# Optimization experiments

Measured on AMD Instinct MI355X. Metric: run time of the kernel, lower is better.

The kernel has to match this reference:

```python
import jax, jax.numpy as jnp
import numpy as np
from jax.scipy.special import gammaln

ADIM, ODIM = 256, 80
B, T_TEXT, T_FEATS = 4, 160, 800


def conv1d(x, w, b, pad):
    # x: (B, C_in, T), w: (C_out, C_in, K)
    y = jax.lax.conv_general_dilated(x, w, (1,), [(pad, pad)],
                                     dimension_numbers=('NCH', 'OIH', 'NCH'))
    return y + b[None, :, None]


def betaln(x, y):
    return gammaln(x) + gammaln(y) - gammaln(x + y)


def beta_binomial_prior(T, N, w=1.0):
    # Matches scipy betabinom.logpmf(k, N, alpha, beta) with
    # alpha = w*arange(1, T+1), beta = w*(T - alpha + 1), k = arange(N).
    a = w * jnp.arange(1, T + 1, dtype=jnp.float32)          # (T,)
    b = w * (T - a + 1.0)                                    # (T,)
    k = jnp.arange(N, dtype=jnp.float32)[:, None]            # (N, 1)
    Nf = jnp.float32(N)
    logp = (gammaln(Nf + 1.0) - gammaln(k + 1.0) - gammaln(Nf - k + 1.0)
            + betaln(k + a, Nf - k + b) - betaln(a, b))      # (N, T)
    return logp.T                                            # (T_feats, T_text)


def setup_inputs() -> dict:
    key = jax.random.key(0)
    ks = jax.random.split(key, 12)
    s = 0.05
    return {
        'text': jax.random.normal(ks[0], (B, T_TEXT, ADIM), jnp.float32),
        'feats': jax.random.normal(ks[1], (B, T_FEATS, ODIM), jnp.float32),
        'text_lengths': jnp.full((B,), T_TEXT, dtype=jnp.int32),
        'feats_lengths': jnp.full((B,), T_FEATS, dtype=jnp.int32),
        'x_masks': jnp.zeros((B, T_TEXT), dtype=bool),
        't_w1': jax.random.normal(ks[2], (ADIM, ADIM, 3), jnp.float32) * s,
        't_b1': jnp.zeros((ADIM,), jnp.float32),
        't_w2': jax.random.normal(ks[3], (ADIM, ADIM, 1), jnp.float32) * s,
        't_b2': jnp.zeros((ADIM,), jnp.float32),
        'f_w1': jax.random.normal(ks[4], (ADIM, ODIM, 3), jnp.float32) * s,
        'f_b1': jnp.zeros((ADIM,), jnp.float32),
        'f_w2': jax.random.normal(ks[5], (ADIM, ADIM, 3), jnp.float32) * s,
        'f_b2': jnp.zeros((ADIM,), jnp.float32),
        'f_w3': jax.random.normal(ks[6], (ADIM, ADIM, 1), jnp.float32) * s,
        'f_b3': jnp.zeros((ADIM,), jnp.float32),
    }


def reference(text, feats, text_lengths, feats_lengths, x_masks,
              t_w1, t_b1, t_w2, t_b2, f_w1, f_b1, f_w2, f_b2, f_w3, f_b3):
    # text conv stem: (B, T_text, adim) -> (B, T_text, adim)
    t = jnp.swapaxes(text, 1, 2)
    t = jax.nn.relu(conv1d(t, t_w1, t_b1, 1))
    t = conv1d(t, t_w2, t_b2, 0)
    t = jnp.swapaxes(t, 1, 2)
    # feats conv stem: (B, T_feats, odim) -> (B, T_feats, adim)
    f = jnp.swapaxes(feats, 1, 2)
    f = jax.nn.relu(conv1d(f, f_w1, f_b1, 1))
    f = jax.nn.relu(conv1d(f, f_w2, f_b2, 1))
    f = conv1d(f, f_w3, f_b3, 0)
    f = jnp.swapaxes(f, 1, 2)
    # L2-distance score: (B, T_feats, T_text)
    diff = f[:, :, None, :] - t[:, None, :, :]               # (B,Tf,Tt,adim)
    score = -jnp.sqrt(jnp.sum(diff * diff, axis=-1))
    score = jnp.where(x_masks[:, None, :], -jnp.inf, score)
    log_p_attn = jax.nn.log_softmax(score, axis=-1)
    # beta-binomial prior (lengths == max, so prior fills the whole matrix)
    prior = beta_binomial_prior(feats.shape[1], text.shape[1])
    return log_p_attn + prior[None, :, :]
```

## Files before the change

kernel.cpp:

```cpp
#include <hip/hip_runtime.h>
#include <math.h>

#define NB 4
#define TTEXT 160
#define TFEAT 800

typedef __bf16 bf16x8 __attribute__((ext_vector_type(8)));
typedef float f32x4 __attribute__((ext_vector_type(4)));

__device__ inline unsigned short f2bf(float f) {
    unsigned int u = __builtin_bit_cast(unsigned int, f);
    unsigned int r = u + 0x7fffu + ((u >> 16) & 1u);
    return (unsigned short)(r >> 16);
}
__device__ inline float bf2f(unsigned short h) {
    unsigned int u = ((unsigned int)h) << 16;
    return __builtin_bit_cast(float, u);
}

__global__ __launch_bounds__(256) void prep_kernel(
    const float* __restrict__ tw1, const float* __restrict__ tw2,
    const float* __restrict__ fw1, const float* __restrict__ fw2,
    const float* __restrict__ fw3,
    unsigned short* __restrict__ wb_t1, unsigned short* __restrict__ wb_t2,
    unsigned short* __restrict__ wb_f1, unsigned short* __restrict__ wb_f2,
    unsigned short* __restrict__ wb_f3, float* __restrict__ lg)
{
    const int u = blockIdx.x * 256 + threadIdx.x;
    if (u >= 598016) {
        const int n = u - 598016;
        if (n < 1024) lg[n] = (n >= 1) ? (float)lgamma((double)n) : 0.0f;
        return;
    }
    int rem = u;
    int CIN, CINP, K; const float* src; unsigned short* dst;
    if (rem < 196608)                  { CIN = 256; CINP = 256; K = 3; src = tw1; dst = wb_t1; }
    else if ((rem -= 196608) < 65536)  { CIN = 256; CINP = 256; K = 1; src = tw2; dst = wb_t2; }
    else if ((rem -= 65536) < 73728)   { CIN = 80;  CINP = 96;  K = 3; src = fw1; dst = wb_f1; }
    else if ((rem -= 73728) < 196608)  { CIN = 256; CINP = 256; K = 3; src = fw2; dst = wb_f2; }
    else { rem -= 196608;                CIN = 256; CINP = 256; K = 1; src = fw3; dst = wb_f3; }
    const int q = rem & 31, coc = rem >> 5, co = coc & 255, c = coc >> 8;
    const int cpk = CINP / 32, k = c / cpk, ci = (c % cpk) * 32 + q;
    const float v = (ci < CIN) ? src[((size_t)co * CIN + ci) * K + k] : 0.0f;
    dst[rem] = f2bf(v);
}

__global__ __launch_bounds__(512) void stems_kernel(
    const float* __restrict__ text, const float* __restrict__ feats,
    const unsigned short* __restrict__ wt1, const float* __restrict__ bt1,
    const unsigned short* __restrict__ wt2, const float* __restrict__ bt2,
    const unsigned short* __restrict__ wf1, const float* __restrict__ bf1v,
    const unsigned short* __restrict__ wf2, const float* __restrict__ bf2v,
    const unsigned short* __restrict__ wf3, const float* __restrict__ bf3v,
    unsigned short* __restrict__ tB, float* __restrict__ tnorm,
    unsigned short* __restrict__ fC, float* __restrict__ fnorm)
{
    __shared__ __align__(16) unsigned short s[11056];
    __shared__ float s_red[16][8];
    const int tid = threadIdx.x;
    const int w  = tid >> 6;
    const int l  = tid & 63;
    const int lr = l & 15;
    const int lk = l >> 4;
    const int co0 = w * 32;
    const int koff = lk * 8;
    const int bid = blockIdx.x;

    if (bid < 40) {
        const int b  = bid & 3;
        const int t0 = (bid >> 2) << 4;
        unsigned short* s_in  = s;
        unsigned short* s_mid = s + 4752;

        for (int idx = tid; idx < 18 * 64; idx += 512) {
            const int r = idx >> 6, c4 = idx & 63;
            const int x = t0 - 1 + r;
            float4 v = {0.f, 0.f, 0.f, 0.f};
            if (x >= 0 && x < TTEXT)
                v = *(const float4*)(text + ((size_t)(b * TTEXT + x)) * 256 + c4 * 4);
            unsigned short* p = s_in + r * 264 + c4 * 4;
            p[0] = f2bf(v.x); p[1] = f2bf(v.y); p[2] = f2bf(v.z); p[3] = f2bf(v.w);
        }
        __syncthreads();

        f32x4 acc[2];
#pragma unroll
        for (int n = 0; n < 2; ++n) acc[n] = {0.f, 0.f, 0.f, 0.f};
#pragma unroll 8
        for (int c = 0; c < 24; ++c) {
            const int k  = c >> 3;
            const int ci = ((c & 7) << 5) + koff;
            const bf16x8 a = *(const bf16x8*)(s_in + (lr + k) * 264 + ci);
#pragma unroll
            for (int n = 0; n < 2; ++n) {
                const bf16x8 bb = *(const bf16x8*)(wt1 + (((size_t)c * 256 + co0 + n * 16 + lr) << 5) + koff);
                acc[n] = __builtin_amdgcn_mfma_f32_16x16x32_bf16(a, bb, acc[n], 0, 0, 0);
            }
        }
#pragma unroll
        for (int n = 0; n < 2; ++n) {
            const float bv = bt1[co0 + n * 16 + lr];
#pragma unroll
            for (int r = 0; r < 4; ++r)
                s_mid[(lk * 4 + r) * 264 + co0 + n * 16 + lr] = f2bf(fmaxf(acc[n][r] + bv, 0.f));
        }
        __syncthreads();

        f32x4 a2[2];
#pragma unroll
        for (int n = 0; n < 2; ++n) a2[n] = {0.f, 0.f, 0.f, 0.f};
#pragma unroll
        for (int c = 0; c < 8; ++c) {
            const bf16x8 a = *(const bf16x8*)(s_mid + lr * 264 + (c << 5) + koff);
#pragma unroll
            for (int n = 0; n < 2; ++n) {
                const bf16x8 bb = *(const bf16x8*)(wt2 + (((size_t)c * 256 + co0 + n * 16 + lr) << 5) + koff);
                a2[n] = __builtin_amdgcn_mfma_f32_16x16x32_bf16(a, bb, a2[n], 0, 0, 0);
            }
        }
        float bv2[2];
#pragma unroll
        for (int n = 0; n < 2; ++n) bv2[n] = bt2[co0 + n * 16 + lr];
#pragma unroll
        for (int r = 0; r < 4; ++r) {
            const int row = lk * 4 + r;
            float np = 0.f;
#pragma unroll
            for (int n = 0; n < 2; ++n) {
                const unsigned short h = f2bf(a2[n][r] + bv2[n]);
                tB[((size_t)(b * TTEXT + t0 + row)) * 256 + co0 + n * 16 + lr] = h;
                const float vq = bf2f(h);
                np = fmaf(vq, vq, np);
            }
            np += __shfl_xor(np, 1);
            np += __shfl_xor(np, 2);
            np += __shfl_xor(np, 4);
            np += __shfl_xor(np, 8);
            if (lr == 0) s_red[row][w] = np;
        }
        __syncthreads();
        if (tid < 16) {
            float s4 = 0.f;
#pragma unroll
            for (int ww = 0; ww < 8; ++ww) s4 += s_red[tid][ww];
            tnorm[b * TTEXT + t0 + tid] = s4;
        }
    } else {
        const int fb = bid - 40;
        const int b  = fb & 3;
        const int t0 = (fb >> 2) << 4;
        unsigned short* s_fin = s;
        unsigned short* s_b1  = s + 2080;
        unsigned short* s_b2  = s + 6832;

        for (int idx = tid; idx < 20 * 24; idx += 512) {
            const int r  = idx / 24, c4 = idx - r * 24;
            const int ch = c4 * 4;
            const int x  = t0 - 2 + r;
            float4 v = {0.f, 0.f, 0.f, 0.f};
            if (ch < 80 && x >= 0 && x < TFEAT)
                v = *(const float4*)(feats + ((size_t)(b * TFEAT + x)) * 80 + ch);
            unsigned short* p = s_fin + r * 104 + ch;
            p[0] = f2bf(v.x); p[1] = f2bf(v.y); p[2] = f2bf(v.z); p[3] = f2bf(v.w);
        }
        __syncthreads();

        f32x4 acc1[2][2];
#pragma unroll
        for (int m = 0; m < 2; ++m)
#pragma unroll
            for (int n = 0; n < 2; ++n) acc1[m][n] = {0.f, 0.f, 0.f, 0.f};
#pragma unroll
        for (int c = 0; c < 9; ++c) {
            const int k  = c / 3;
            const int ci = (c - k * 3) * 32 + koff;
            bf16x8 a[2];
#pragma unroll
            for (int m = 0; m < 2; ++m) {
                int rr = m * 16 + lr + k;
                if (rr > 19) rr = 19;
                a[m] = *(const bf16x8*)(s_fin + rr * 104 + ci);
            }
#pragma unroll
            for (int n = 0; n < 2; ++n) {
                const bf16x8 bb = *(const bf16x8*)(wf1 + (((size_t)c * 256 + co0 + n * 16 + lr) << 5) + koff);
                acc1[0][n] = __builtin_amdgcn_mfma_f32_16x16x32_bf16(a[0], bb, acc1[0][n], 0, 0, 0);
                acc1[1][n] = __builtin_amdgcn_mfma_f32_16x16x32_bf16(a[1], bb, acc1[1][n], 0, 0, 0);
            }
        }
#pragma unroll
        for (int n = 0; n < 2; ++n) {
            const float bv = bf1v[co0 + n * 16 + lr];
#pragma unroll
            for (int m = 0; m < 2; ++m)
#pragma unroll
                for (int r = 0; r < 4; ++r) {
                    const int i = m * 16 + lk * 4 + r;
                    if (i < 18)
                        s_b1[i * 264 + co0 + n * 16 + lr] = f2bf(fmaxf(acc1[m][n][r] + bv, 0.f));
                }
        }
        __syncthreads();

        f32x4 acc2[2];
#pragma unroll
        for (int n = 0; n < 2; ++n) acc2[n] = {0.f, 0.f, 0.f, 0.f};
#pragma unroll 8
        for (int c = 0; c < 24; ++c) {
            const int k  = c >> 3;
            const int ci = ((c & 7) << 5) + koff;
            const bf16x8 a = *(const bf16x8*)(s_b1 + (lr + k) * 264 + ci);
#pragma unroll
            for (int n = 0; n < 2; ++n) {
                const bf16x8 bb = *(const bf16x8*)(wf2 + (((size_t)c * 256 + co0 + n * 16 + lr) << 5) + koff);
                acc2[n] = __builtin_amdgcn_mfma_f32_16x16x32_bf16(a, bb, acc2[n], 0, 0, 0);
            }
        }
#pragma unroll
        for (int n = 0; n < 2; ++n) {
            const float bv = bf2v[co0 + n * 16 + lr];
#pragma unroll
            for (int r = 0; r < 4; ++r)
                s_b2[(lk * 4 + r) * 264 + co0 + n * 16 + lr] = f2bf(fmaxf(acc2[n][r] + bv, 0.f));
        }
        __syncthreads();

        f32x4 a3[2];
#pragma unroll
        for (int n = 0; n < 2; ++n) a3[n] = {0.f, 0.f, 0.f, 0.f};
#pragma unroll
        for (int c = 0; c < 8; ++c) {
            const bf16x8 a = *(const bf16x8*)(s_b2 + lr * 264 + (c << 5) + koff);
#pragma unroll
            for (int n = 0; n < 2; ++n) {
                const bf16x8 bb = *(const bf16x8*)(wf3 + (((size_t)c * 256 + co0 + n * 16 + lr) << 5) + koff);
                a3[n] = __builtin_amdgcn_mfma_f32_16x16x32_bf16(a, bb, a3[n], 0, 0, 0);
            }
        }
        float bv3[2];
#pragma unroll
        for (int n = 0; n < 2; ++n) bv3[n] = bf3v[co0 + n * 16 + lr];
#pragma unroll
        for (int r = 0; r < 4; ++r) {
            const int row = lk * 4 + r;
            float np = 0.f;
#pragma unroll
            for (int n = 0; n < 2; ++n) {
                const unsigned short h = f2bf(a3[n][r] + bv3[n]);
                fC[((size_t)(b * TFEAT + t0 + row)) * 256 + co0 + n * 16 + lr] = h;
                const float vq = bf2f(h);
                np = fmaf(vq, vq, np);
            }
            np += __shfl_xor(np, 1);
            np += __shfl_xor(np, 2);
            np += __shfl_xor(np, 4);
            np += __shfl_xor(np, 8);
            if (lr == 0) s_red[row][w] = np;
        }
        __syncthreads();
        if (tid < 16) {
            float s4 = 0.f;
#pragma unroll
            for (int ww = 0; ww < 8; ++ww) s4 += s_red[tid][ww];
            fnorm[b * TFEAT + t0 + tid] = s4;
        }
    }
}

__global__ __launch_bounds__(256) void score_mfma(
    const unsigned short* __restrict__ F, const unsigned short* __restrict__ Tt,
    const float* __restrict__ fnorm, const float* __restrict__ tnorm,
    const unsigned char* __restrict__ xmask, const float* __restrict__ lg,
    float* __restrict__ out)
{
    const int b  = blockIdx.y;
    const int tid = threadIdx.x;
    const int w  = tid >> 6;
    const int l  = tid & 63;
    const int lr = l & 15;
    const int lk = l >> 4;
    const int i0 = blockIdx.x * 16;
    const int nstart = (w < 2) ? w * 3 : 6 + (w - 2) * 2;
    const int ncnt   = (w < 2) ? 3 : 2;

    __shared__ float s_red[16][4];
    __shared__ float s_red2[16][4];

    f32x4 acc[3];
#pragma unroll
    for (int ni = 0; ni < 3; ++ni) acc[ni] = {0.f, 0.f, 0.f, 0.f};

    const unsigned short* __restrict__ Fp = F + ((size_t)(b * TFEAT + i0 + lr)) * 256;
    const unsigned short* __restrict__ Tp = Tt + ((size_t)b * TTEXT) * 256;

#pragma unroll
    for (int c = 0; c < 8; ++c) {
        const int d = c * 32 + lk * 8;
        const bf16x8 a = *(const bf16x8*)(Fp + d);
#pragma unroll
        for (int ni = 0; ni < 3; ++ni) {
            if (ni < ncnt) {
                const int n = nstart + ni;
                const bf16x8 bb = *(const bf16x8*)(Tp + ((size_t)(n * 16 + lr)) * 256 + d);
                acc[ni] = __builtin_amdgcn_mfma_f32_16x16x32_bf16(a, bb, acc[ni], 0, 0, 0);
            }
        }
    }

    float fn[4];
#pragma unroll
    for (int r = 0; r < 4; ++r) fn[r] = fnorm[b * TFEAT + i0 + lk * 4 + r];
    float tn[3]; bool mk[3];
#pragma unroll
    for (int ni = 0; ni < 3; ++ni) {
        const int j = (nstart + ni) * 16 + lr;
        if (ni < ncnt) {
            tn[ni] = tnorm[b * TTEXT + j];
            mk[ni] = xmask[b * TTEXT + j] != 0;
        } else { tn[ni] = 0.f; mk[ni] = true; }
    }
    float sc[3][4];
#pragma unroll
    for (int ni = 0; ni < 3; ++ni)
#pragma unroll
        for (int r = 0; r < 4; ++r) {
            const float d2 = fn[r] + tn[ni] - 2.0f * acc[ni][r];
            const float sv = -sqrtf(fmaxf(d2, 0.0f));
            sc[ni][r] = mk[ni] ? -INFINITY : sv;
        }

#pragma unroll
    for (int r = 0; r < 4; ++r) {
        float mx = sc[0][r];
#pragma unroll
        for (int ni = 1; ni < 3; ++ni) mx = fmaxf(mx, sc[ni][r]);
        mx = fmaxf(mx, __shfl_xor(mx, 1));
        mx = fmaxf(mx, __shfl_xor(mx, 2));
        mx = fmaxf(mx, __shfl_xor(mx, 4));
        mx = fmaxf(mx, __shfl_xor(mx, 8));
        if (lr == 0) s_red[lk * 4 + r][w] = mx;
    }
    __syncthreads();
    float gmax[4];
#pragma unroll
    for (int r = 0; r < 4; ++r) {
        const int row = lk * 4 + r;
        gmax[r] = fmaxf(fmaxf(s_red[row][0], s_red[row][1]),
                        fmaxf(s_red[row][2], s_red[row][3]));
        float sm = 0.f;
#pragma unroll
        for (int ni = 0; ni < 3; ++ni)
            if (ni < ncnt) sm += expf(sc[ni][r] - gmax[r]);
        sm += __shfl_xor(sm, 1);
        sm += __shfl_xor(sm, 2);
        sm += __shfl_xor(sm, 4);
        sm += __shfl_xor(sm, 8);
        if (lr == 0) s_red2[row][w] = sm;
    }
    __syncthreads();

    const float cst = lg[161] - lg[961] + lg[801];
#pragma unroll
    for (int r = 0; r < 4; ++r) {
        const int row = lk * 4 + r;
        const float lse = gmax[r] + logf(s_red2[row][0] + s_red2[row][1]
                                       + s_red2[row][2] + s_red2[row][3]);
        const int grow = i0 + row;
        const float rowterm = cst - lg[grow + 1] - lg[801 - grow];
#pragma unroll
        for (int ni = 0; ni < 3; ++ni) {
            if (ni < ncnt) {
                const int j = (nstart + ni) * 16 + lr;
                const float prior = rowterm - lg[j + 1] - lg[160 - j]
                                  + lg[grow + j + 1] + lg[960 - grow - j];
                out[((size_t)(b * TFEAT + grow)) * TTEXT + j] = sc[ni][r] - lse + prior;
            }
        }
    }
}

extern "C" void kernel_launch(void* const* d_in, const int* in_sizes, int n_in,
                              void* d_out, int out_size, void* d_ws, size_t ws_size,
                              hipStream_t stream) {
    const float* text  = (const float*)d_in[0];
    const float* feats = (const float*)d_in[1];
    const unsigned char* xmask = (const unsigned char*)d_in[4];
    const float* t_w1 = (const float*)d_in[5];
    const float* t_b1 = (const float*)d_in[6];
    const float* t_w2 = (const float*)d_in[7];
    const float* t_b2 = (const float*)d_in[8];
    const float* f_w1 = (const float*)d_in[9];
    const float* f_b1 = (const float*)d_in[10];
    const float* f_w2 = (const float*)d_in[11];
    const float* f_b2 = (const float*)d_in[12];
    const float* f_w3 = (const float*)d_in[13];
    const float* f_b3 = (const float*)d_in[14];
    float* out = (float*)d_out;

    char* wp = (char*)d_ws;
    auto alloc = [&](size_t bytes) -> void* {
        void* p = wp; wp += (bytes + 255) & ~(size_t)255; return p;
    };
    float* lg = (float*)alloc(1024 * 4);
    unsigned short* wb_t1 = (unsigned short*)alloc(196608 * 2);
    unsigned short* wb_t2 = (unsigned short*)alloc(65536 * 2);
    unsigned short* wb_f1 = (unsigned short*)alloc(73728 * 2);
    unsigned short* wb_f2 = (unsigned short*)alloc(196608 * 2);
    unsigned short* wb_f3 = (unsigned short*)alloc(65536 * 2);
    unsigned short* tB = (unsigned short*)alloc((size_t)NB * TTEXT * 256 * 2);
    unsigned short* fC = (unsigned short*)alloc((size_t)NB * TFEAT * 256 * 2);
    float* fnorm = (float*)alloc((size_t)NB * TFEAT * 4);
    float* tnorm = (float*)alloc((size_t)NB * TTEXT * 4);

    prep_kernel<<<2340, 256, 0, stream>>>(
        t_w1, t_w2, f_w1, f_w2, f_w3, wb_t1, wb_t2, wb_f1, wb_f2, wb_f3, lg);

    stems_kernel<<<240, 512, 0, stream>>>(
        text, feats,
        wb_t1, t_b1, wb_t2, t_b2,
        wb_f1, f_b1, wb_f2, f_b2, wb_f3, f_b3,
        tB, tnorm, fC, fnorm);

    score_mfma<<<dim3(50, NB), 256, 0, stream>>>(fC, tB, fnorm, tnorm, xmask, lg, out);
}
```

Before: 35.92 us.

## Fuse score computation into stems kernel with per-batch spin-wait flags

Merges the score/log-softmax kernel into the stems kernel. Each feats block keeps its projected features and norms in shared memory and waits on a per-batch atomic counter until the 10 text blocks for that batch have published tB and tnorm. This removes one kernel launch and the global round trip for fC and fnorm. The cost is a spin-wait that only works if all 240 blocks are co-resident; otherwise it can deadlock or stall.

```diff
diff --git a/kernel.cpp b/kernel.cpp
--- a/kernel.cpp
+++ b/kernel.cpp
@@ -24,8 +24,10 @@
     const float* __restrict__ fw3,
     unsigned short* __restrict__ wb_t1, unsigned short* __restrict__ wb_t2,
     unsigned short* __restrict__ wb_f1, unsigned short* __restrict__ wb_f2,
-    unsigned short* __restrict__ wb_f3, float* __restrict__ lg)
+    unsigned short* __restrict__ wb_f3, float* __restrict__ lg,
+    int* __restrict__ flags)
 {
+    if (blockIdx.x == 0 && threadIdx.x < 16) flags[threadIdx.x] = 0;
     const int u = blockIdx.x * 256 + threadIdx.x;
     if (u >= 598016) {
         const int n = u - 598016;
@@ -45,18 +47,22 @@
     dst[rem] = f2bf(v);
 }
 
-__global__ __launch_bounds__(512) void stems_kernel(
+__global__ __launch_bounds__(512) void fused_kernel(
     const float* __restrict__ text, const float* __restrict__ feats,
+    const unsigned char* __restrict__ xmask,
     const unsigned short* __restrict__ wt1, const float* __restrict__ bt1,
     const unsigned short* __restrict__ wt2, const float* __restrict__ bt2,
     const unsigned short* __restrict__ wf1, const float* __restrict__ bf1v,
     const unsigned short* __restrict__ wf2, const float* __restrict__ bf2v,
     const unsigned short* __restrict__ wf3, const float* __restrict__ bf3v,
+    const float* __restrict__ lg,
     unsigned short* __restrict__ tB, float* __restrict__ tnorm,
-    unsigned short* __restrict__ fC, float* __restrict__ fnorm)
+    int* __restrict__ flags, float* __restrict__ out)
 {
     __shared__ __align__(16) unsigned short s[11056];
     __shared__ float s_red[16][8];
+    __shared__ float s_red2[16][8];
+    __shared__ float s_fn[16];
     const int tid = threadIdx.x;
     const int w  = tid >> 6;
     const int l  = tid & 63;
@@ -145,162 +151,154 @@
             for (int ww = 0; ww < 8; ++ww) s4 += s_red[tid][ww];
             tnorm[b * TTEXT + t0 + tid] = s4;
         }
-    } else {
-        const int fb = bid - 40;
-        const int b  = fb & 3;
-        const int t0 = (fb >> 2) << 4;
-        unsigned short* s_fin = s;
-        unsigned short* s_b1  = s + 2080;
-        unsigned short* s_b2  = s + 6832;
-
-        for (int idx = tid; idx < 20 * 24; idx += 512) {
-            const int r  = idx / 24, c4 = idx - r * 24;
-            const int ch = c4 * 4;
-            const int x  = t0 - 2 + r;
-            float4 v = {0.f, 0.f, 0.f, 0.f};
-            if (ch < 80 && x >= 0 && x < TFEAT)
-                v = *(const float4*)(feats + ((size_t)(b * TFEAT + x)) * 80 + ch);
-            unsigned short* p = s_fin + r * 104 + ch;
-            p[0] = f2bf(v.x); p[1] = f2bf(v.y); p[2] = f2bf(v.z); p[3] = f2bf(v.w);
-        }
         __syncthreads();
-
-        f32x4 acc1[2][2];
+        __threadfence();
+        if (tid == 0) atomicAdd(&flags[b], 1);
+        return;
+    }
+
+    const int fb = bid - 40;
+    const int b  = fb & 3;
+    const int t0 = (fb >> 2) << 4;
+    unsigned short* s_fin = s;
+    unsigned short* s_b1  = s + 2080;
+    unsigned short* s_b2  = s + 6832;
+    unsigned short* s_out = s;
+
+    for (int idx = tid; idx < 20 * 24; idx += 512) {
+        const int r  = idx / 24, c4 = idx - r * 24;
+        const int ch = c4 * 4;
+        const int x  = t0 - 2 + r;
+        float4 v = {0.f, 0.f, 0.f, 0.f};
+        if (ch < 80 && x >= 0 && x < TFEAT)
+            v = *(const float4*)(feats + ((size_t)(b * TFEAT + x)) * 80 + ch);
+        unsigned short* p = s_fin + r * 104 + ch;
+        p[0] = f2bf(v.x); p[1] = f2bf(v.y); p[2] = f2bf(v.z); p[3] = f2bf(v.w);
+    }
+    __syncthreads();
+
+    f32x4 acc1[2][2];
+#pragma unroll
+    for (int m = 0; m < 2; ++m)
+#pragma unroll
+        for (int n = 0; n < 2; ++n) acc1[m][n] = {0.f, 0.f, 0.f, 0.f};
+#pragma unroll
+    for (int c = 0; c < 9; ++c) {
+        const int k  = c / 3;
+        const int ci = (c - k * 3) * 32 + koff;
+        bf16x8 a[2];
+#pragma unroll
+        for (int m = 0; m < 2; ++m) {
+            int rr = m * 16 + lr + k;
+            if (rr > 19) rr = 19;
+            a[m] = *(const bf16x8*)(s_fin + rr * 104 + ci);
+        }
+#pragma unroll
+        for (int n = 0; n < 2; ++n) {
+            const bf16x8 bb = *(const bf16x8*)(wf1 + (((size_t)c * 256 + co0 + n * 16 + lr) << 5) + koff);
+            acc1[0][n] = __builtin_amdgcn_mfma_f32_16x16x32_bf16(a[0], bb, acc1[0][n], 0, 0, 0);
+            acc1[1][n] = __builtin_amdgcn_mfma_f32_16x16x32_bf16(a[1], bb, acc1[1][n], 0, 0, 0);
+        }
+    }
+#pragma unroll
+    for (int n = 0; n < 2; ++n) {
+        const float bv = bf1v[co0 + n * 16 + lr];
 #pragma unroll
         for (int m = 0; m < 2; ++m)
 #pragma unroll
-            for (int n = 0; n < 2; ++n) acc1[m][n] = {0.f, 0.f, 0.f, 0.f};
-#pragma unroll
-        for (int c = 0; c < 9; ++c) {
-            const int k  = c / 3;
-            const int ci = (c - k * 3) * 32 + koff;
-            bf16x8 a[2];
-#pragma unroll
-            for (int m = 0; m < 2; ++m) {
-                int rr = m * 16 + lr + k;
-                if (rr > 19) rr = 19;
-                a[m] = *(const bf16x8*)(s_fin + rr * 104 + ci);
-            }
-#pragma unroll
-            for (int n = 0; n < 2; ++n) {
-                const bf16x8 bb = *(const bf16x8*)(wf1 + (((size_t)c * 256 + co0 + n * 16 + lr) << 5) + koff);
-                acc1[0][n] = __builtin_amdgcn_mfma_f32_16x16x32_bf16(a[0], bb, acc1[0][n], 0, 0, 0);
-                acc1[1][n] = __builtin_amdgcn_mfma_f32_16x16x32_bf16(a[1], bb, acc1[1][n], 0, 0, 0);
-            }
-        }
+            for (int r = 0; r < 4; ++r) {
+                const int i = m * 16 + lk * 4 + r;
+                if (i < 18)
+                    s_b1[i * 264 + co0 + n * 16 + lr] = f2bf(fmaxf(acc1[m][n][r] + bv, 0.f));
+            }
+    }
+    __syncthreads();
+
+    f32x4 acc2[2];
+#pragma unroll
+    for (int n = 0; n < 2; ++n) acc2[n] = {0.f, 0.f, 0.f, 0.f};
+#pragma unroll 8
+    for (int c = 0; c < 24; ++c) {
+        const int k  = c >> 3;
+        const int ci = ((c & 7) << 5) + koff;
+        const bf16x8 a = *(const bf16x8*)(s_b1 + (lr + k) * 264 + ci);
 #pragma unroll
         for (int n = 0; n < 2; ++n) {
-            const float bv = bf1v[co0 + n * 16 + lr];
-#pragma unroll
-            for (int m = 0; m < 2; ++m)
-#pragma unroll
-                for (int r = 0; r < 4; ++r) {
-                    const int i = m * 16 + lk * 4 + r;
-                    if (i < 18)
-                        s_b1[i * 264 + co0 + n * 16 + lr] = f2bf(fmaxf(acc1[m][n][r] + bv, 0.f));
-                }
-        }
-        __syncthreads();
-
-        f32x4 acc2[2];
-#pragma unroll
-        for (int n = 0; n < 2; ++n) acc2[n] = {0.f, 0.f, 0.f, 0.f};
-#pragma unroll 8
-        for (int c = 0; c < 24; ++c) {
-            const int k  = c >> 3;
-            const int ci = ((c & 7) << 5) + koff;
-            const bf16x8 a = *(const bf16x8*)(s_b1 + (lr + k) * 264 + ci);
-#pragma unroll
-            for (int n = 0; n < 2; ++n) {
-                const bf16x8 bb = *(const bf16x8*)(wf2 + (((size_t)c * 256 + co0 + n * 16 + lr) << 5) + koff);
-                acc2[n] = __builtin_amdgcn_mfma_f32_16x16x32_bf16(a, bb, acc2[n], 0, 0, 0);
-            }
-        }
+            const bf16x8 bb = *(const bf16x8*)(wf2 + (((size_t)c * 256 + co0 + n * 16 + lr) << 5) + koff);
+            acc2[n] = __builtin_amdgcn_mfma_f32_16x16x32_bf16(a, bb, acc2[n], 0, 0, 0);
+        }
+    }
+#pragma unroll
+    for (int n = 0; n < 2; ++n) {
+        const float bv = bf2v[co0 + n * 16 + lr];
+#pragma unroll
+        for (int r = 0; r < 4; ++r)
+            s_b2[(lk * 4 + r) * 264 + co0 + n * 16 + lr] = f2bf(fmaxf(acc2[n][r] + bv, 0.f));
+    }
+    __syncthreads();
+
+    f32x4 a3[2];
+#pragma unroll
+    for (int n = 0; n < 2; ++n) a3[n] = {0.f, 0.f, 0.f, 0.f};
+#pragma unroll
+    for (int c = 0; c < 8; ++c) {
+        const bf16x8 a = *(const bf16x8*)(s_b2 + lr * 264 + (c << 5) + koff);
 #pragma unroll
         for (int n = 0; n < 2; ++n) {
-            const float bv = bf2v[co0 + n * 16 + lr];
-#pragma unroll
-            for (int r = 0; r < 4; ++r)
-                s_b2[(lk * 4 + r) * 264 + co0 + n * 16 + lr] = f2bf(fmaxf(acc2[n][r] + bv, 0.f));
-        }
-        __syncthreads();
-
-        f32x4 a3[2];
-#pragma unroll
-        for (int n = 0; n < 2; ++n) a3[n] = {0.f, 0.f, 0.f, 0.f};
-#pragma unroll
-        for (int c = 0; c < 8; ++c) {
-            const bf16x8 a = *(const bf16x8*)(s_b2 + lr * 264 + (c << 5) + koff);
-#pragma unroll
-            for (int n = 0; n < 2; ++n) {
-                const bf16x8 bb = *(const bf16x8*)(wf3 + (((size_t)c * 256 + co0 + n * 16 + lr) << 5) + koff);
-                a3[n] = __builtin_amdgcn_mfma_f32_16x16x32_bf16(a, bb, a3[n], 0, 0, 0);
-            }
-        }
-        float bv3[2];
-#pragma unroll
-        for (int n = 0; n < 2; ++n) bv3[n] = bf3v[co0 + n * 16 + lr];
-#pragma unroll
-        for (int r = 0; r < 4; ++r) {
-            const int row = lk * 4 + r;
-            float np = 0.f;
-#pragma unroll
-            for (int n = 0; n < 2; ++n) {
-                const unsigned short h = f2bf(a3[n][r] + bv3[n]);
-                fC[((size_t)(b * TFEAT + t0 + row)) * 256 + co0 + n * 16 + lr] = h;
-                const float vq = bf2f(h);
-                np = fmaf(vq, vq, np);
-            }
-            np += __shfl_xor(np, 1);
-            np += __shfl_xor(np, 2);
-            np += __shfl_xor(np, 4);
-            np += __shfl_xor(np, 8);
-            if (lr == 0) s_red[row][w] = np;
-        }
-        __syncthreads();
-        if (tid < 16) {
-            float s4 = 0.f;
-#pragma unroll
-            for (int ww = 0; ww < 8; ++ww) s4 += s_red[tid][ww];
-            fnorm[b * TFEAT + t0 + tid] = s4;
-        }
-    }
-}
-
-__global__ __launch_bounds__(256) void score_mfma(
-    const unsigned short* __restrict__ F, const unsigned short* __restrict__ Tt,
-    const float* __restrict__ fnorm, const float* __restrict__ tnorm,
-    const unsigned char* __restrict__ xmask, const float* __restrict__ lg,
-    float* __restrict__ out)
-{
-    const int b  = blockIdx.y;
-    const int tid = threadIdx.x;
-    const int w  = tid >> 6;
-    const int l  = tid & 63;
-    const int lr = l & 15;
-    const int lk = l >> 4;
-    const int i0 = blockIdx.x * 16;
-    const int nstart = (w < 2) ? w * 3 : 6 + (w - 2) * 2;
-    const int ncnt   = (w < 2) ? 3 : 2;
-
-    __shared__ float s_red[16][4];
-    __shared__ float s_red2[16][4];
-
-    f32x4 acc[3];
-#pragma unroll
-    for (int ni = 0; ni < 3; ++ni) acc[ni] = {0.f, 0.f, 0.f, 0.f};
-
-    const unsigned short* __restrict__ Fp = F + ((size_t)(b * TFEAT + i0 + lr)) * 256;
-    const unsigned short* __restrict__ Tp = Tt + ((size_t)b * TTEXT) * 256;
+            const bf16x8 bb = *(const bf16x8*)(wf3 + (((size_t)c * 256 + co0 + n * 16 + lr) << 5) + koff);
+            a3[n] = __builtin_amdgcn_mfma_f32_16x16x32_bf16(a, bb, a3[n], 0, 0, 0);
+        }
+    }
+    float bv3[2];
+#pragma unroll
+    for (int n = 0; n < 2; ++n) bv3[n] = bf3v[co0 + n * 16 + lr];
+#pragma unroll
+    for (int r = 0; r < 4; ++r) {
+        const int row = lk * 4 + r;
+        float np = 0.f;
+#pragma unroll
+        for (int n = 0; n < 2; ++n) {
+            const unsigned short h = f2bf(a3[n][r] + bv3[n]);
+            s_out[row * 264 + co0 + n * 16 + lr] = h;
+            const float vq = bf2f(h);
+            np = fmaf(vq, vq, np);
+        }
+        np += __shfl_xor(np, 1);
+        np += __shfl_xor(np, 2);
+        np += __shfl_xor(np, 4);
+        np += __shfl_xor(np, 8);
+        if (lr == 0) s_red[row][w] = np;
+    }
+    __syncthreads();
+    if (tid < 16) {
+        float s4 = 0.f;
+#pragma unroll
+        for (int ww = 0; ww < 8; ++ww) s4 += s_red[tid][ww];
+        s_fn[tid] = s4;
+    }
+
+    if (tid == 0) {
+        while (atomicAdd(&flags[b], 0) < 10) __builtin_amdgcn_s_sleep(2);
+    }
+    __syncthreads();
+    __threadfence();
+
+    const int NI = (w < 2) ? 2 : 1;
+    const int i0 = t0;
+
+    f32x4 acc[2];
+#pragma unroll
+    for (int ni = 0; ni < 2; ++ni) acc[ni] = {0.f, 0.f, 0.f, 0.f};
+    const unsigned short* __restrict__ Tp = tB + ((size_t)b * TTEXT) * 256;
 
 #pragma unroll
     for (int c = 0; c < 8; ++c) {
-        const int d = c * 32 + lk * 8;
-        const bf16x8 a = *(const bf16x8*)(Fp + d);
-#pragma unroll
-        for (int ni = 0; ni < 3; ++ni) {
-            if (ni < ncnt) {
-                const int n = nstart + ni;
+        const int d = c * 32 + koff;
+        const bf16x8 a = *(const bf16x8*)(s_out + lr * 264 + d);
+#pragma unroll
+        for (int ni = 0; ni < 2; ++ni) {
+            if (ni < NI) {
+                const int n = w + ni * 8;
                 const bf16x8 bb = *(const bf16x8*)(Tp + ((size_t)(n * 16 + lr)) * 256 + d);
                 acc[ni] = __builtin_amdgcn_mfma_f32_16x16x32_bf16(a, bb, acc[ni], 0, 0, 0);
             }
@@ -309,19 +307,19 @@
 
     float fn[4];
 #pragma unroll
-    for (int r = 0; r < 4; ++r) fn[r] = fnorm[b * TFEAT + i0 + lk * 4 + r];
-    float tn[3]; bool mk[3];
-#pragma unroll
-    for (int ni = 0; ni < 3; ++ni) {
-        const int j = (nstart + ni) * 16 + lr;
-        if (ni < ncnt) {
+    for (int r = 0; r < 4; ++r) fn[r] = s_fn[lk * 4 + r];
+    float tn[2]; bool mk[2];
+#pragma unroll
+    for (int ni = 0; ni < 2; ++ni) {
+        if (ni < NI) {
+            const int j = (w + ni * 8) * 16 + lr;
             tn[ni] = tnorm[b * TTEXT + j];
             mk[ni] = xmask[b * TTEXT + j] != 0;
         } else { tn[ni] = 0.f; mk[ni] = true; }
     }
-    float sc[3][4];
-#pragma unroll
-    for (int ni = 0; ni < 3; ++ni)
+    float sc[2][4];
+#pragma unroll
+    for (int ni = 0; ni < 2; ++ni)
 #pragma unroll
         for (int r = 0; r < 4; ++r) {
             const float d2 = fn[r] + tn[ni] - 2.0f * acc[ni][r];
@@ -331,9 +329,7 @@
 
 #pragma unroll
     for (int r = 0; r < 4; ++r) {
-        float mx = sc[0][r];
-#pragma unroll
-        for (int ni = 1; ni < 3; ++ni) mx = fmaxf(mx, sc[ni][r]);
+        float mx = fmaxf(sc[0][r], sc[1][r]);
         mx = fmaxf(mx, __shfl_xor(mx, 1));
         mx = fmaxf(mx, __shfl_xor(mx, 2));
         mx = fmaxf(mx, __shfl_xor(mx, 4));
@@ -345,12 +341,14 @@
 #pragma unroll
     for (int r = 0; r < 4; ++r) {
         const int row = lk * 4 + r;
-        gmax[r] = fmaxf(fmaxf(s_red[row][0], s_red[row][1]),
-                        fmaxf(s_red[row][2], s_red[row][3]));
+        float g = s_red[row][0];
+#pragma unroll
+        for (int ww = 1; ww < 8; ++ww) g = fmaxf(g, s_red[row][ww]);
+        gmax[r] = g;
         float sm = 0.f;
 #pragma unroll
-        for (int ni = 0; ni < 3; ++ni)
-            if (ni < ncnt) sm += expf(sc[ni][r] - gmax[r]);
+        for (int ni = 0; ni < 2; ++ni)
+            if (ni < NI) sm += expf(sc[ni][r] - g);
         sm += __shfl_xor(sm, 1);
         sm += __shfl_xor(sm, 2);
         sm += __shfl_xor(sm, 4);
@@ -363,14 +361,16 @@
 #pragma unroll
     for (int r = 0; r < 4; ++r) {
         const int row = lk * 4 + r;
-        const float lse = gmax[r] + logf(s_red2[row][0] + s_red2[row][1]
-                                       + s_red2[row][2] + s_red2[row][3]);
+        float ssum = s_red2[row][0];
+#pragma unroll
+        for (int ww = 1; ww < 8; ++ww) ssum += s_red2[row][ww];
+        const float lse = gmax[r] + logf(ssum);
         const int grow = i0 + row;
         const float rowterm = cst - lg[grow + 1] - lg[801 - grow];
 #pragma unroll
-        for (int ni = 0; ni < 3; ++ni) {
-            if (ni < ncnt) {
-                const int j = (nstart + ni) * 16 + lr;
+        for (int ni = 0; ni < 2; ++ni) {
+            if (ni < NI) {
+                const int j = (w + ni * 8) * 16 + lr;
                 const float prior = rowterm - lg[j + 1] - lg[160 - j]
                                   + lg[grow + j + 1] + lg[960 - grow - j];
                 out[((size_t)(b * TFEAT + grow)) * TTEXT + j] = sc[ni][r] - lse + prior;
@@ -408,18 +408,15 @@
     unsigned short* wb_f2 = (unsigned short*)alloc(196608 * 2);
     unsigned short* wb_f3 = (unsigned short*)alloc(65536 * 2);
     unsigned short* tB = (unsigned short*)alloc((size_t)NB * TTEXT * 256 * 2);
-    unsigned short* fC = (unsigned short*)alloc((size_t)NB * TFEAT * 256 * 2);
-    float* fnorm = (float*)alloc((size_t)NB * TFEAT * 4);
     float* tnorm = (float*)alloc((size_t)NB * TTEXT * 4);
+    int* flags = (int*)alloc(64);
 
     prep_kernel<<<2340, 256, 0, stream>>>(
-        t_w1, t_w2, f_w1, f_w2, f_w3, wb_t1, wb_t2, wb_f1, wb_f2, wb_f3, lg);
-
-    stems_kernel<<<240, 512, 0, stream>>>(
-        text, feats,
+        t_w1, t_w2, f_w1, f_w2, f_w3, wb_t1, wb_t2, wb_f1, wb_f2, wb_f3, lg, flags);
+
+    fused_kernel<<<240, 512, 0, stream>>>(
+        text, feats, xmask,
         wb_t1, t_b1, wb_t2, t_b2,
         wb_f1, f_b1, wb_f2, f_b2, wb_f3, f_b3,
-        tB, tnorm, fC, fnorm);
-
-    score_mfma<<<dim3(50, NB), 256, 0, stream>>>(fC, tB, fnorm, tnorm, xmask, lg, out);
+        lg, tB, tnorm, flags, out);
 }
```

Measured after the change: 61.33 us. +70.7%, slower.
